# Kernel tuning notes

Measured on AMD Instinct MI355X. Metric: run time of the kernel, lower is better.

Reference implementation:

```python
import jax, jax.numpy as jnp
import numpy as np

N = 768                       # atoms
E = N * (N - 1)               # complete directed graph edges
DIM = 64                      # hidden dim
CUT = 5.0                     # rbf high
NC = 50                       # n_centers = ceil(5/0.1)
ODIM = 1                      # output_dim
NCONV = 3
_centers_np = np.linspace(0.0, CUT, NC)
CENTERS = jnp.asarray(_centers_np, jnp.float32)
GAP = float(_centers_np[1] - _centers_np[0])
RO_IN = 2 * ODIM + NC         # readout input: 2*output_dim + rbf fan_out = 52


def softplus_bt(x, beta, thr):
    # torch.nn.Softplus(beta, threshold): linear above threshold
    bx = beta * x
    return jnp.where(bx > thr, x, jax.nn.softplus(bx) / beta)


def rbf(d):
    # exp(-(1/gap) * (d - mu_k)^2); d: (..., 1) -> (..., NC)
    return jnp.exp((-1.0 / GAP) * (d - CENTERS) ** 2)


def setup_inputs() -> dict:
    key = jax.random.key(0)
    ks = jax.random.split(key, 24)
    atom_types = jax.random.randint(ks[0], (N,), 0, 100)
    edge_distances = jax.random.uniform(ks[1], (E, 1), jnp.float32) * CUT
    # complete directed graph, edge order matches the nested i,j loop (i!=j)
    ii = np.repeat(np.arange(N), N)
    jj = np.tile(np.arange(N), N)
    m = ii != jj
    src = jnp.asarray(ii[m], jnp.int32)
    dst = jnp.asarray(jj[m], jnp.int32)

    def p(k, shape, fan):
        return jax.random.normal(k, shape, jnp.float32) / np.sqrt(fan)

    embedding = p(ks[2], (100, DIM), DIM).at[0].set(0.0)  # padding_idx=0
    L = NCONV
    return {
        'atom_types': atom_types, 'edge_distances': edge_distances,
        'src': src, 'dst': dst, 'embedding': embedding,
        'w1': p(ks[3], (L, DIM, DIM), DIM),                 # node_layer1 (no bias)
        'pw1': p(ks[4], (L, NC, DIM), NC), 'pb1': p(ks[5], (L, DIM), NC),
        'pw2': p(ks[6], (L, DIM, DIM), DIM), 'pb2': p(ks[7], (L, DIM), DIM),
        'qw1': p(ks[8], (L, DIM, DIM), DIM), 'qb1': p(ks[9], (L, DIM), DIM),
        'qw2': p(ks[10], (L, DIM, DIM), DIM), 'qb2': p(ks[11], (L, DIM), DIM),
        'au_w1': p(ks[12], (DIM, 64), DIM), 'au_b1': p(ks[13], (64,), DIM),
        'au_w2': p(ks[14], (64, ODIM), 64), 'au_b2': p(ks[15], (ODIM,), 64),
        'ro_w1': p(ks[16], (RO_IN, 64), RO_IN), 'ro_b1': p(ks[17], (64,), RO_IN),
        'ro_w2': p(ks[18], (64, 2), 64), 'ro_b2': p(ks[19], (2,), 64),
    }


def reference(atom_types, edge_distances, src, dst, embedding,
              w1, pw1, pb1, pw2, pb2, qw1, qb1, qw2, qb2,
              au_w1, au_b1, au_w2, au_b2, ro_w1, ro_b1, ro_w2, ro_b2):
    h = embedding[atom_types]                       # (N, DIM)
    rbf_out = rbf(edge_distances)                   # (E, NC)
    for l in range(NCONV):
        nw = h @ w1[l]                              # node weights (N, DIM)
        e = softplus_bt(rbf_out @ pw1[l] + pb1[l], 0.5, 14) @ pw2[l] + pb2[l]  # (E, DIM)
        msg = nw[src] * e                           # gather-mul (E, DIM)
        agg = jax.ops.segment_sum(msg, dst, num_segments=N)  # scatter-sum (N, DIM)
        upd = softplus_bt(agg @ qw1[l] + qb1[l], 0.5, 14) @ qw2[l] + qb2[l]
        h = h + upd
    # atom_update with ShiftSoftplus (beta=1, shift=2, threshold=20)
    ha = softplus_bt(h @ au_w1 + au_b1, 1.0, 20) - jnp.log(jnp.float32(2.0))
    ha = ha @ au_w2 + au_b2                         # (N, ODIM)
    # readout over all ordered pairs i!=j, in edge order == (src, dst)
    edge_feat = jnp.concatenate([ha[src], ha[dst], rbf_out], axis=-1)  # (E, 52)
    logits = jax.nn.relu(edge_feat @ ro_w1 + ro_b1) @ ro_w2 + ro_b2    # (E, 2)
    return jax.nn.softmax(logits, axis=-1)
```

## Files before the change

kernel.cpp:

```cpp
#include <hip/hip_runtime.h>
#include <hip/hip_fp16.h>

#define NATOMS 768
#define NM1    767
#define NEDGE  (768*767)
#define DIM    64
#define NC     50
#define GAPF   (5.0f/49.0f)
#define NIGAP  (-49.0f/5.0f)
#define G      512
#define STEPF  (5.0f/511.0f)
#define INVSTEP (511.0f/5.0f)
#define LN2F   0.693147180559945f

#define WS_H     0
#define WS_NWA   49152
#define WS_NWB   73728
#define WS_HA    98304
#define WS_DISTT 99328
#define WS_TT    689152

#define TBL_BYTES   131072
#define CONV_SMEM   (TBL_BYTES + 16*3*64*4 + 3*192*4)

__device__ __forceinline__ float softplus05(float x) {
    float bx = 0.5f * x;
    return (bx > 14.0f) ? x : 2.0f * __logf(1.0f + __expf(bx));
}
__device__ __forceinline__ int lane_bcast_i(int v, int l) {
    return __builtin_amdgcn_readlane(v, l);
}
__device__ __forceinline__ float lane_bcast_f(float v, int l) {
    return __uint_as_float((unsigned)__builtin_amdgcn_readlane((int)__float_as_uint(v), l));
}

__global__ __launch_bounds__(256)
void k_pre(const int* __restrict__ types, const float* __restrict__ dist,
           const float* __restrict__ emb, const float* __restrict__ w1all,
           const float* __restrict__ pw1, const float* __restrict__ pb1,
           const float* __restrict__ pw2, const float* __restrict__ pb2,
           const float* __restrict__ row1, const float* __restrict__ rob1,
           float* __restrict__ ws) {
    __shared__ float s_t[4 * 64];
    const int tid = threadIdx.x, widx = tid >> 6, c = tid & 63;
    float*  h     = ws + WS_H;
    __half* nwh   = (__half*)(ws + WS_NWA);
    float*  distT = ws + WS_DISTT;
    __half* TTh   = (__half*)(ws + WS_TT);
    const int b = blockIdx.x;

    if (b < 512) {
        const int w = b * 4 + widx, tbl = w >> 9, g = w & 511;
        const float d = g * STEPF;
        float val;
        if (tbl < 3) {
            const float* W1 = pw1 + tbl * NC * DIM;
            float t1 = pb1[tbl * DIM + c];
            for (int k = 0; k < NC; ++k) {
                float x = d - GAPF * (float)k;
                t1 = fmaf(__expf(NIGAP * x * x), W1[k * DIM + c], t1);
            }
            s_t[widx * 64 + c] = softplus05(t1);
            const float* W2 = pw2 + tbl * DIM * DIM;
            val = pb2[tbl * DIM + c];
            #pragma unroll 8
            for (int k = 0; k < DIM; ++k)
                val = fmaf(s_t[widx * 64 + k], W2[k * DIM + c], val);
        } else {
            val = rob1[c];
            for (int k = 0; k < NC; ++k) {
                float x = d - GAPF * (float)k;
                val = fmaf(__expf(NIGAP * x * x), row1[(2 + k) * DIM + c], val);
            }
        }
        __half* TTt = TTh + tbl * (G * DIM * 2);
        TTt[(g * DIM + c) * 2] = __float2half(val);
        if (g > 0) TTt[((g - 1) * DIM + c) * 2 + 1] = __float2half(val);
    } else if (b < 704) {
        const int i = (b - 512) * 4 + widx;
        float hv = emb[types[i] * DIM + c];
        h[i * DIM + c] = hv;
        s_t[widx * 64 + c] = hv;
        float acc = 0.0f;
        #pragma unroll 8
        for (int k = 0; k < DIM; ++k)
            acc = fmaf(s_t[widx * 64 + k], w1all[k * DIM + c], acc);
        nwh[i * DIM + c] = __float2half(acc);
    } else {
        const int idx = (b - 704) * 256 + tid;
        const int j = idx / NATOMS, i = idx - j * NATOMS;
        distT[idx] = (i == j) ? 0.0f : dist[i * NM1 + (j - (j > i))];
    }
}

__global__ __launch_bounds__(1024)
void k_edgeupd_lds(const __half2* __restrict__ TTl, const float* __restrict__ distT,
                   const __half* __restrict__ nwin,
                   const float* __restrict__ qw1, const float* __restrict__ qb1,
                   const float* __restrict__ qw2, const float* __restrict__ qb2,
                   float* __restrict__ h,
                   const float* __restrict__ wnext, __half* __restrict__ nwout,
                   const float* __restrict__ auw1, const float* __restrict__ aub1,
                   const float* __restrict__ auw2, const float* __restrict__ aub2,
                   float* __restrict__ ha, int last) {
    extern __shared__ char smem[];
    float* s_part = (float*)(smem + TBL_BYTES);
    float* s_updA = (float*)(smem + TBL_BYTES + 12288);
    const int tid = threadIdx.x, widx = tid >> 6, c = tid & 63;
    const int j0 = blockIdx.x * 3;
    const int s0 = widx * 48;

    {
        const float4* src4 = (const float4*)TTl;
        float4* dst4 = (float4*)smem;
        #pragma unroll
        for (int k = 0; k < 8; ++k) dst4[tid + k * 1024] = src4[tid + k * 1024];
    }
    __syncthreads();

    const int cS = (c < 48) ? c : 47;
    float dA = distT[j0 * NATOMS + s0 + cS];
    float dB = distT[(j0 + 1) * NATOMS + s0 + cS];
    float dC = distT[(j0 + 2) * NATOMS + s0 + cS];
    float pA = dA * INVSTEP, pB = dB * INVSTEP, pC = dC * INVSTEP;
    int gA = (int)pA, gB = (int)pB, gC = (int)pC;
    gA = (gA < 0) ? 0 : ((gA > 510) ? 510 : gA);
    gB = (gB < 0) ? 0 : ((gB > 510) ? 510 : gB);
    gC = (gC < 0) ? 0 : ((gC > 510) ? 510 : gC);
    float fA = pA - (float)gA, fB = pB - (float)gB, fC = pC - (float)gC;
    int kA = gA * 256, kB = gB * 256, kC = gC * 256;

    const char* Tb = (const char*)smem + c * 4;
    float acc0 = 0.0f, acc1 = 0.0f, acc2 = 0.0f;
    #pragma unroll 8
    for (int it = 0; it < 48; ++it) {
        float nwv = __half2float(nwin[(s0 + it) * DIM + c]);
        {
            float2 tt = __half22float2(*(const __half2*)(Tb + lane_bcast_i(kA, it)));
            float e = fmaf(lane_bcast_f(fA, it), tt.y - tt.x, tt.x);
            acc0 = fmaf(e, nwv, acc0);
        }
        {
            float2 tt = __half22float2(*(const __half2*)(Tb + lane_bcast_i(kB, it)));
            float e = fmaf(lane_bcast_f(fB, it), tt.y - tt.x, tt.x);
            acc1 = fmaf(e, nwv, acc1);
        }
        {
            float2 tt = __half22float2(*(const __half2*)(Tb + lane_bcast_i(kC, it)));
            float e = fmaf(lane_bcast_f(fC, it), tt.y - tt.x, tt.x);
            acc2 = fmaf(e, nwv, acc2);
        }
    }
    s_part[(widx * 3 + 0) * 64 + c] = acc0;
    s_part[(widx * 3 + 1) * 64 + c] = acc1;
    s_part[(widx * 3 + 2) * 64 + c] = acc2;
    __syncthreads();

    if (widx < 3) {
        const int jt = j0 + widx;
        float tot = 0.0f;
        #pragma unroll
        for (int w16 = 0; w16 < 16; ++w16) tot += s_part[(w16 * 3 + widx) * 64 + c];
        float2 t0 = __half22float2(*(const __half2*)Tb);
        tot -= t0.x * __half2float(nwin[jt * DIM + c]);
        float* su = s_updA + widx * 192;
        su[c] = tot;
        float t = qb1[c];
        #pragma unroll 8
        for (int k = 0; k < DIM; ++k) t = fmaf(su[k], qw1[k * DIM + c], t);
        su[64 + c] = softplus05(t);
        float o = qb2[c];
        #pragma unroll 8
        for (int k = 0; k < DIM; ++k) o = fmaf(su[64 + k], qw2[k * DIM + c], o);
        float hn = h[jt * DIM + c] + o;
        h[jt * DIM + c] = hn;
        su[128 + c] = hn;
        if (!last) {
            float v = 0.0f;
            #pragma unroll 8
            for (int k = 0; k < DIM; ++k) v = fmaf(su[128 + k], wnext[k * DIM + c], v);
            nwout[jt * DIM + c] = __float2half(v);
        } else {
            float t2 = aub1[c];
            #pragma unroll 8
            for (int k = 0; k < DIM; ++k) t2 = fmaf(su[128 + k], auw1[k * DIM + c], t2);
            t2 = ((t2 > 20.0f) ? t2 : __logf(1.0f + __expf(t2))) - LN2F;
            float v = t2 * auw2[c];
            #pragma unroll
            for (int s = 32; s > 0; s >>= 1) v += __shfl_down(v, s, 64);
            if (c == 0) ha[jt] = v + aub2[0];
        }
    }
}

__global__ __launch_bounds__(512)
void k_edgeupd(const __half2* __restrict__ TTl, const float* __restrict__ distT,
               const __half* __restrict__ nwin,
               const float* __restrict__ qw1, const float* __restrict__ qb1,
               const float* __restrict__ qw2, const float* __restrict__ qb2,
               float* __restrict__ h,
               const float* __restrict__ wnext, __half* __restrict__ nwout,
               const float* __restrict__ auw1, const float* __restrict__ aub1,
               const float* __restrict__ auw2, const float* __restrict__ aub2,
               float* __restrict__ ha, int last) {
    __shared__ float s_part[8][64];
    __shared__ float s_upd[192];
    const int tid = threadIdx.x, widx = tid >> 6, c = tid & 63;
    const int j = blockIdx.x;
    const int s0 = widx * 96;

    const char* TTb = (const char*)TTl + c * 4;
    float csum = 0.0f;
    {
        float d = distT[j * NATOMS + s0 + c];
        float pos = d * INVSTEP;
        int g = (int)pos;
        g = (g < 0) ? 0 : ((g > 510) ? 510 : g);
        float f = pos - (float)g;
        int kx = g * 256;
        #pragma unroll 8
        for (int it = 0; it < 64; ++it) {
            int kxu = lane_bcast_i(kx, it);
            float fu = lane_bcast_f(f, it);
            float2 tt = __half22float2(*(const __half2*)(TTb + kxu));
            float e = fmaf(fu, tt.y - tt.x, tt.x);
            float nwv = __half2float(nwin[(s0 + it) * DIM + c]);
            csum = fmaf(e, nwv, csum);
        }
    }
    {
        float d = distT[j * NATOMS + s0 + 64 + (c & 31)];
        float pos = d * INVSTEP;
        int g = (int)pos;
        g = (g < 0) ? 0 : ((g > 510) ? 510 : g);
        float f = pos - (float)g;
        int kx = g * 256;
        #pragma unroll 8
        for (int it = 0; it < 32; ++it) {
            int kxu = lane_bcast_i(kx, it);
            float fu = lane_bcast_f(f, it);
            float2 tt = __half22float2(*(const __half2*)(TTb + kxu));
            float e = fmaf(fu, tt.y - tt.x, tt.x);
            float nwv = __half2float(nwin[(s0 + 64 + it) * DIM + c]);
            csum = fmaf(e, nwv, csum);
        }
    }
    s_part[widx][c] = csum;
    __syncthreads();

    if (widx == 0) {
        float tot = 0.0f;
        #pragma unroll
        for (int w8 = 0; w8 < 8; ++w8) tot += s_part[w8][c];
        float2 t0 = __half22float2(*(const __half2*)TTb);
        tot -= t0.x * __half2float(nwin[j * DIM + c]);
        s_upd[c] = tot;
        float t = qb1[c];
        #pragma unroll 8
        for (int k = 0; k < DIM; ++k) t = fmaf(s_upd[k], qw1[k * DIM + c], t);
        s_upd[64 + c] = softplus05(t);
        float o = qb2[c];
        #pragma unroll 8
        for (int k = 0; k < DIM; ++k) o = fmaf(s_upd[64 + k], qw2[k * DIM + c], o);
        float hn = h[j * DIM + c] + o;
        h[j * DIM + c] = hn;
        s_upd[128 + c] = hn;
        if (!last) {
            float v = 0.0f;
            #pragma unroll 8
            for (int k = 0; k < DIM; ++k) v = fmaf(s_upd[128 + k], wnext[k * DIM + c], v);
            nwout[j * DIM + c] = __float2half(v);
        } else {
            float t2 = aub1[c];
            #pragma unroll 8
            for (int k = 0; k < DIM; ++k) t2 = fmaf(s_upd[128 + k], auw1[k * DIM + c], t2);
            t2 = ((t2 > 20.0f) ? t2 : __logf(1.0f + __expf(t2))) - LN2F;
            float v = t2 * auw2[c];
            #pragma unroll
            for (int s = 32; s > 0; s >>= 1) v += __shfl_down(v, s, 64);
            if (c == 0) ha[j] = v + aub2[0];
        }
    }
}

__global__ __launch_bounds__(256)
void k_ro(const float* __restrict__ dist, const int* __restrict__ src,
          const int* __restrict__ dst, const float* __restrict__ ha,
          const __half2* __restrict__ TTro,
          const float* __restrict__ row1, const float* __restrict__ row2,
          const float* __restrict__ rob2, float* __restrict__ out) {
    __shared__ float4 s_pre[4][64];
    __shared__ float s_h[4][16 * 65];
    __shared__ float s_w2[128];
    const int tid = threadIdx.x, widx = tid >> 6, c = tid & 63;
    if (tid < 128) s_w2[tid] = row2[tid];
    __syncthreads();
    const int ebase = (blockIdx.x * 4 + widx) * 64;
    {
        int eg = ebase + c;
        float d = dist[eg];
        float pos = d * INVSTEP;
        int kk = (int)pos;
        kk = (kk < 0) ? 0 : ((kk > 510) ? 510 : kk);
        float fa = ha[src[eg]], fb = ha[dst[eg]];
        s_pre[widx][c] = make_float4(__int_as_float(kk * 256), pos - (float)kk, fa, fb);
    }
    const char* TTb2 = (const char*)TTro + c * 4;
    const float wa = row1[c], wb = row1[DIM + c];
    const int e2 = (c >> 1) & 15, p2 = c & 1, kh = c >> 5;
    const float bias2 = (kh == 0) ? rob2[p2] : 0.0f;
    float* sh = s_h[widx];
    #pragma unroll
    for (int ch = 0; ch < 4; ++ch) {
        #pragma unroll 4
        for (int e = 0; e < 16; ++e) {
            float4 p = s_pre[widx][ch * 16 + e];
            float2 tt = __half22float2(*(const __half2*)(TTb2 + __float_as_int(p.x)));
            float hv = fmaf(p.y, tt.y - tt.x, tt.x);
            hv = fmaf(p.z, wa, hv);
            hv = fmaf(p.w, wb, hv);
            sh[e * 65 + c] = fmaxf(hv, 0.0f);
        }
        float lsum = bias2;
        #pragma unroll 8
        for (int k8 = 0; k8 < 32; ++k8) {
            int k = kh * 32 + k8;
            lsum = fmaf(sh[e2 * 65 + k], s_w2[2 * k + p2], lsum);
        }
        lsum += __shfl_xor(lsum, 32, 64);
        float other = __shfl_xor(lsum, 1, 64);
        float m = fmaxf(lsum, other);
        float ea = __expf(lsum - m), eb = __expf(other - m);
        float r = ea / (ea + eb);
        if (c < 32) out[ebase * 2 + ch * 32 + c] = r;
    }
}

extern "C" void kernel_launch(void* const* d_in, const int* in_sizes, int n_in,
                              void* d_out, int out_size, void* d_ws, size_t ws_size,
                              hipStream_t stream) {
    const int*   types = (const int*)d_in[0];
    const float* dist  = (const float*)d_in[1];
    const int*   srcI  = (const int*)d_in[2];
    const int*   dstI  = (const int*)d_in[3];
    const float* emb   = (const float*)d_in[4];
    const float* w1    = (const float*)d_in[5];
    const float* pw1   = (const float*)d_in[6];
    const float* pb1   = (const float*)d_in[7];
    const float* pw2   = (const float*)d_in[8];
    const float* pb2   = (const float*)d_in[9];
    const float* qw1   = (const float*)d_in[10];
    const float* qb1   = (const float*)d_in[11];
    const float* qw2   = (const float*)d_in[12];
    const float* qb2   = (const float*)d_in[13];
    const float* auw1  = (const float*)d_in[14];
    const float* aub1  = (const float*)d_in[15];
    const float* auw2  = (const float*)d_in[16];
    const float* aub2  = (const float*)d_in[17];
    const float* row1  = (const float*)d_in[18];
    const float* rob1  = (const float*)d_in[19];
    const float* row2  = (const float*)d_in[20];
    const float* rob2  = (const float*)d_in[21];

    float* ws   = (float*)d_ws;
    float* outp = (float*)d_out;
    const __half2* TT = (const __half2*)(ws + WS_TT);
    __half* nwbuf[2] = { (__half*)(ws + WS_NWA), (__half*)(ws + WS_NWB) };

    int ldsOK = 0;
    {
        int dev = 0, maxLds = 0;
        if (hipGetDevice(&dev) == hipSuccess &&
            hipDeviceGetAttribute(&maxLds,
                hipDeviceAttributeMaxSharedMemoryPerMultiprocessor, dev) == hipSuccess &&
            maxLds >= CONV_SMEM &&
            hipFuncSetAttribute((const void*)k_edgeupd_lds,
                hipFuncAttributeMaxDynamicSharedMemorySize,
                CONV_SMEM) == hipSuccess)
            ldsOK = 1;
    }

    k_pre<<<3008, 256, 0, stream>>>(types, dist, emb, w1, pw1, pb1, pw2, pb2,
                                    row1, rob1, ws);
    for (int l = 0; l < 3; ++l) {
        if (ldsOK) {
            k_edgeupd_lds<<<256, 1024, CONV_SMEM, stream>>>(TT + l * (G * DIM),
                ws + WS_DISTT, nwbuf[l & 1],
                qw1 + l * DIM * DIM, qb1 + l * DIM,
                qw2 + l * DIM * DIM, qb2 + l * DIM,
                ws + WS_H,
                (l < 2) ? (w1 + (l + 1) * DIM * DIM) : w1, nwbuf[(l + 1) & 1],
                auw1, aub1, auw2, aub2, ws + WS_HA, (l == 2) ? 1 : 0);
        } else {
            k_edgeupd<<<768, 512, 0, stream>>>(TT + l * (G * DIM),
                ws + WS_DISTT, nwbuf[l & 1],
                qw1 + l * DIM * DIM, qb1 + l * DIM,
                qw2 + l * DIM * DIM, qb2 + l * DIM,
                ws + WS_H,
                (l < 2) ? (w1 + (l + 1) * DIM * DIM) : w1, nwbuf[(l + 1) & 1],
                auw1, aub1, auw2, aub2, ws + WS_HA, (l == 2) ? 1 : 0);
        }
    }
    k_ro<<<2301, 256, 0, stream>>>(dist, srcI, dstI, ws + WS_HA, TT + 3 * (G * DIM),
                                   row1, row2, rob2, outp);
}
```

Before: 191.7 us.

## Stage halved readout lookup table in LDS with persistent 1024-thread readout kernel

The readout rbf@W1 lookup table is shrunk from 512 to 256 grid points so it fits in 64 KiB, and a new readout kernel copies it into LDS once per block. The kernel then runs 256 persistent 1024-thread blocks over the edges, instead of 2301 small blocks each gathering from the global table. This is meant to replace scattered global/L2 table reads with LDS reads and to cut launch/block overhead. The coarser table grid adds linear-interpolation error to the readout pre-activations.

```diff
diff --git a/kernel.cpp b/kernel.cpp
--- a/kernel.cpp
+++ b/kernel.cpp
@@ -11,6 +11,8 @@
 #define G      512
 #define STEPF  (5.0f/511.0f)
 #define INVSTEP (511.0f/5.0f)
+#define ROSTEP (5.0f/255.0f)
+#define ROINV  (255.0f/5.0f)
 #define LN2F   0.693147180559945f
 
 #define WS_H     0
@@ -22,6 +24,8 @@
 
 #define TBL_BYTES   131072
 #define CONV_SMEM   (TBL_BYTES + 16*3*64*4 + 3*192*4)
+#define RO_TBL      65536
+#define RO_SMEM     (RO_TBL + 16*64*16 + 16*16*65*4 + 512)
 
 __device__ __forceinline__ float softplus05(float x) {
     float bx = 0.5f * x;
@@ -51,9 +55,8 @@
 
     if (b < 512) {
         const int w = b * 4 + widx, tbl = w >> 9, g = w & 511;
-        const float d = g * STEPF;
-        float val;
         if (tbl < 3) {
+            const float d = g * STEPF;
             const float* W1 = pw1 + tbl * NC * DIM;
             float t1 = pb1[tbl * DIM + c];
             for (int k = 0; k < NC; ++k) {
@@ -62,20 +65,24 @@
             }
             s_t[widx * 64 + c] = softplus05(t1);
             const float* W2 = pw2 + tbl * DIM * DIM;
-            val = pb2[tbl * DIM + c];
+            float val = pb2[tbl * DIM + c];
             #pragma unroll 8
             for (int k = 0; k < DIM; ++k)
                 val = fmaf(s_t[widx * 64 + k], W2[k * DIM + c], val);
-        } else {
-            val = rob1[c];
+            __half* TTt = TTh + tbl * (G * DIM * 2);
+            TTt[(g * DIM + c) * 2] = __float2half(val);
+            if (g > 0) TTt[((g - 1) * DIM + c) * 2 + 1] = __float2half(val);
+        } else if (g < 256) {
+            const float d = g * ROSTEP;
+            float val = rob1[c];
             for (int k = 0; k < NC; ++k) {
                 float x = d - GAPF * (float)k;
                 val = fmaf(__expf(NIGAP * x * x), row1[(2 + k) * DIM + c], val);
             }
-        }
-        __half* TTt = TTh + tbl * (G * DIM * 2);
-        TTt[(g * DIM + c) * 2] = __float2half(val);
-        if (g > 0) TTt[((g - 1) * DIM + c) * 2 + 1] = __float2half(val);
+            __half* TTt = TTh + 3 * (G * DIM * 2);
+            TTt[(g * DIM + c) * 2] = __float2half(val);
+            if (g > 0) TTt[((g - 1) * DIM + c) * 2 + 1] = __float2half(val);
+        }
     } else if (b < 704) {
         const int i = (b - 512) * 4 + widx;
         float hv = emb[types[i] * DIM + c];
@@ -283,6 +290,74 @@
     }
 }
 
+__global__ __launch_bounds__(1024)
+void k_ro_lds(const float* __restrict__ dist, const int* __restrict__ src,
+              const int* __restrict__ dst, const float* __restrict__ ha,
+              const __half2* __restrict__ TTro,
+              const float* __restrict__ row1, const float* __restrict__ row2,
+              const float* __restrict__ rob2, float* __restrict__ out) {
+    extern __shared__ char smem[];
+    float4* s_pre = (float4*)(smem + RO_TBL);
+    float*  s_hA  = (float*)(smem + RO_TBL + 16384);
+    float*  s_w2  = (float*)(smem + RO_TBL + 16384 + 66560);
+    const int tid = threadIdx.x, widx = tid >> 6, c = tid & 63;
+
+    {
+        const float4* s4 = (const float4*)TTro;
+        float4* d4 = (float4*)smem;
+        #pragma unroll
+        for (int k = 0; k < 4; ++k) d4[tid + k * 1024] = s4[tid + k * 1024];
+    }
+    if (tid < 128) s_w2[tid] = row2[tid];
+    __syncthreads();
+
+    const char* Tb = (const char*)smem + c * 4;
+    const float wa = row1[c], wb = row1[DIM + c];
+    const int e2 = (c >> 1) & 15, p2 = c & 1, kh = c >> 5;
+    const float bias2 = (kh == 0) ? rob2[p2] : 0.0f;
+    float* sh = s_hA + widx * (16 * 65);
+    float4* spre = s_pre + widx * 64;
+
+    for (int rnd = 0; rnd < 3; ++rnd) {
+        const int w4 = rnd * 4096 + blockIdx.x * 16 + widx;
+        if (w4 >= 9204) break;
+        const int ebase = w4 * 64;
+        {
+            int eg = ebase + c;
+            float d = dist[eg];
+            float pos = d * ROINV;
+            int kk = (int)pos;
+            kk = (kk < 0) ? 0 : ((kk > 254) ? 254 : kk);
+            float fa = ha[src[eg]], fb = ha[dst[eg]];
+            spre[c] = make_float4(__int_as_float(kk * 256), pos - (float)kk, fa, fb);
+        }
+        #pragma unroll
+        for (int ch = 0; ch < 4; ++ch) {
+            #pragma unroll 4
+            for (int e = 0; e < 16; ++e) {
+                float4 p = spre[ch * 16 + e];
+                float2 tt = __half22float2(*(const __half2*)(Tb + __float_as_int(p.x)));
+                float hv = fmaf(p.y, tt.y - tt.x, tt.x);
+                hv = fmaf(p.z, wa, hv);
+                hv = fmaf(p.w, wb, hv);
+                sh[e * 65 + c] = fmaxf(hv, 0.0f);
+            }
+            float lsum = bias2;
+            #pragma unroll 8
+            for (int k8 = 0; k8 < 32; ++k8) {
+                int k = kh * 32 + k8;
+                lsum = fmaf(sh[e2 * 65 + k], s_w2[2 * k + p2], lsum);
+            }
+            lsum += __shfl_xor(lsum, 32, 64);
+            float other = __shfl_xor(lsum, 1, 64);
+            float m = fmaxf(lsum, other);
+            float ea = __expf(lsum - m), eb = __expf(other - m);
+            float r = ea / (ea + eb);
+            if (c < 32) out[ebase * 2 + ch * 32 + c] = r;
+        }
+    }
+}
+
 __global__ __launch_bounds__(256)
 void k_ro(const float* __restrict__ dist, const int* __restrict__ src,
           const int* __restrict__ dst, const float* __restrict__ ha,
@@ -299,9 +374,9 @@
     {
         int eg = ebase + c;
         float d = dist[eg];
-        float pos = d * INVSTEP;
+        float pos = d * ROINV;
         int kk = (int)pos;
-        kk = (kk < 0) ? 0 : ((kk > 510) ? 510 : kk);
+        kk = (kk < 0) ? 0 : ((kk > 254) ? 254 : kk);
         float fa = ha[src[eg]], fb = ha[dst[eg]];
         s_pre[widx][c] = make_float4(__int_as_float(kk * 256), pos - (float)kk, fa, fb);
     }
@@ -367,23 +442,27 @@
     const __half2* TT = (const __half2*)(ws + WS_TT);
     __half* nwbuf[2] = { (__half*)(ws + WS_NWA), (__half*)(ws + WS_NWB) };
 
-    int ldsOK = 0;
+    int convOK = 0, roOK = 0;
     {
         int dev = 0, maxLds = 0;
         if (hipGetDevice(&dev) == hipSuccess &&
             hipDeviceGetAttribute(&maxLds,
-                hipDeviceAttributeMaxSharedMemoryPerMultiprocessor, dev) == hipSuccess &&
-            maxLds >= CONV_SMEM &&
-            hipFuncSetAttribute((const void*)k_edgeupd_lds,
-                hipFuncAttributeMaxDynamicSharedMemorySize,
-                CONV_SMEM) == hipSuccess)
-            ldsOK = 1;
+                hipDeviceAttributeMaxSharedMemoryPerMultiprocessor, dev) == hipSuccess) {
+            if (maxLds >= CONV_SMEM &&
+                hipFuncSetAttribute((const void*)k_edgeupd_lds,
+                    hipFuncAttributeMaxDynamicSharedMemorySize, CONV_SMEM) == hipSuccess)
+                convOK = 1;
+            if (maxLds >= RO_SMEM &&
+                hipFuncSetAttribute((const void*)k_ro_lds,
+                    hipFuncAttributeMaxDynamicSharedMemorySize, RO_SMEM) == hipSuccess)
+                roOK = 1;
+        }
     }
 
     k_pre<<<3008, 256, 0, stream>>>(types, dist, emb, w1, pw1, pb1, pw2, pb2,
                                     row1, rob1, ws);
     for (int l = 0; l < 3; ++l) {
-        if (ldsOK) {
+        if (convOK) {
             k_edgeupd_lds<<<256, 1024, CONV_SMEM, stream>>>(TT + l * (G * DIM),
                 ws + WS_DISTT, nwbuf[l & 1],
                 qw1 + l * DIM * DIM, qb1 + l * DIM,
@@ -401,6 +480,13 @@
                 auw1, aub1, auw2, aub2, ws + WS_HA, (l == 2) ? 1 : 0);
         }
     }
-    k_ro<<<2301, 256, 0, stream>>>(dist, srcI, dstI, ws + WS_HA, TT + 3 * (G * DIM),
-                                   row1, row2, rob2, outp);
-}
+    if (roOK) {
+        k_ro_lds<<<256, 1024, RO_SMEM, stream>>>(dist, srcI, dstI, ws + WS_HA,
+                                                 TT + 3 * (G * DIM),
+                                                 row1, row2, rob2, outp);
+    } else {
+        k_ro<<<2301, 256, 0, stream>>>(dist, srcI, dstI, ws + WS_HA,
+                                       TT + 3 * (G * DIM),
+                                       row1, row2, rob2, outp);
+    }
+}
```

Result: slower. 206.2 us (+7.5%).
